# Kernel tuning notes

Measured on AMD Instinct MI355X. Metric: run time of the kernel, lower is better.

## Reference

```python
import math
import jax, jax.numpy as jnp
import numpy as np

STRIDE = 8
IMG = 2048
NA = 9            # num anchors per cell (len(cfg['anchor_size']))
NC = 80           # num classes
TOPK = 1000
CONF = 0.05
NMS_T = 0.6
CTR_CLAMP = 32.0
EXP_CLAMP = math.log(1e8)            # DEFAULT_EXP_CLAMP
SCALE_CLAMP = math.log(1000.0 / 16)  # DEFAULT_SCALE_CLAMP


def setup_inputs() -> dict:
    key = jax.random.key(0)
    k1, k2, k3 = jax.random.split(key, 3)
    H = W = IMG // STRIDE  # 256
    obj_pred = jax.random.normal(k1, (1, NA, H, W), jnp.float32)
    cls_pred = jax.random.normal(k2, (1, NA * NC, H, W), jnp.float32)
    reg_pred = jax.random.normal(k3, (1, NA * 4, H, W), jnp.float32) * 0.5
    # generate_anchors: grid centers (+0.5)*stride, tiled anchor sizes -> [H*W*NA, 4] (cx,cy,w,h)
    ys, xs = jnp.meshgrid(jnp.arange(H), jnp.arange(W), indexing='ij')
    xy = (jnp.stack([xs, ys], -1).reshape(-1, 2).astype(jnp.float32) + 0.5) * STRIDE
    sizes = jnp.array([[32, 32], [64, 64], [128, 128], [32, 64], [64, 128],
                       [128, 256], [64, 32], [128, 64], [256, 128]], jnp.float32)
    anchor_boxes = jnp.concatenate(
        [jnp.repeat(xy[:, None, :], NA, axis=1),
         jnp.broadcast_to(sizes[None], (H * W, NA, 2))], axis=-1).reshape(-1, 4)
    return {"obj_pred": obj_pred, "cls_pred": cls_pred,
            "reg_pred": reg_pred, "anchor_boxes": anchor_boxes}


def _detect(obj_pred, cls_pred, reg_pred, anchor_boxes):
    B, _, H, W = obj_pred.shape
    obj = obj_pred.reshape(B, NA, 1, H, W)
    cls = cls_pred.reshape(B, NA, NC, H, W)
    # normalized_cls_pred = cls + obj - log(1 + exp(clamp(cls)) + exp(clamp(obj)))
    norm = cls + obj - jnp.log(1.0 + jnp.exp(jnp.minimum(cls, EXP_CLAMP))
                               + jnp.exp(jnp.minimum(obj, EXP_CLAMP)))
    norm = norm.transpose(0, 3, 4, 1, 2).reshape(B, -1, NC)[0]          # [M, NC]
    reg = reg_pred.reshape(B, NA, 4, H, W).transpose(0, 3, 4, 1, 2).reshape(B, -1, 4)[0]  # [M, 4]
    prob = jax.nn.sigmoid(norm)
    scores_all = prob.max(axis=-1)
    labels_all = prob.argmax(axis=-1)
    scores, idx = jax.lax.top_k(scores_all, TOPK)                        # descending
    labels = labels_all[idx]
    reg = reg[idx]
    anc = anchor_boxes[idx]
    # decode_boxes
    ctr_off = jnp.clip(reg[..., :2] * anc[..., 2:], -CTR_CLAMP, CTR_CLAMP)
    ctr = anc[..., :2] + ctr_off
    wh = anc[..., 2:] * jnp.exp(jnp.minimum(reg[..., 2:], SCALE_CLAMP))
    boxes = jnp.concatenate([ctr - 0.5 * wh, ctr + 0.5 * wh], axis=-1)
    boxes = jnp.clip(boxes / IMG, 0.0, 1.0)
    return scores, labels, boxes


def _nms_keep(scores, labels, boxes):
    # scores are sorted descending; per-class greedy NMS == class-masked global greedy NMS
    valid = scores >= CONF
    x1, y1, x2, y2 = boxes[:, 0], boxes[:, 1], boxes[:, 2], boxes[:, 3]
    areas = (x2 - x1) * (y2 - y1)
    xx1 = jnp.maximum(x1[:, None], x1[None, :])
    yy1 = jnp.maximum(y1[:, None], y1[None, :])
    xx2 = jnp.minimum(x2[:, None], x2[None, :])
    yy2 = jnp.minimum(y2[:, None], y2[None, :])
    inter = jnp.maximum(1e-28, xx2 - xx1) * jnp.maximum(1e-28, yy2 - yy1)
    iou = inter / (areas[:, None] + areas[None, :] - inter + 1e-14)      # [N, N]
    sup = (iou > NMS_T) & (labels[:, None] == labels[None, :])
    later = jnp.arange(TOPK)[None, :] > jnp.arange(TOPK)[:, None]

    def body(i, keep):
        row = sup[i] & later[i] & keep[i]   # i suppresses only if still kept
        return keep & ~row

    return jax.lax.fori_loop(0, TOPK, body, valid)


def reference(obj_pred, cls_pred, reg_pred, anchor_boxes):
    scores, labels, boxes = _detect(obj_pred, cls_pred, reg_pred, anchor_boxes)
    keep = _nms_keep(scores, labels, boxes)
    # fixed-shape outputs: detections sorted by score with a keep mask
    return scores, labels, boxes, keep
```

## Files before the change

### kernel.cpp

```cpp
#include <hip/hip_runtime.h>
#include <stdint.h>

#define NA 9
#define NC 80
#define NTOT 589824
#define NT4  147456
#define TOPK 1000
#define CONF 0.05f
#define NMS_T 0.6
#define CTR_CLAMP 32.0
#define IMGF 2048.0
#define SCALE_CLAMP 4.135166556742356

#define HIST_OFF   4718592u
#define CNT_OFF    4784128u
#define BARC_OFF   4784384u
#define FLAG_OFF   4792576u
#define INITF_OFF  4800768u
#define CAND_OFF   4802816u
#define BOXES_OFF  4835584u
#define LABS_OFF   4851584u
#define SUPB_OFF   4855584u

#define NBLK 512
#define PER_BLK 288
#define SPIN_CAP 200000
#define INIT_MAGIC 0x9E3779B97F4A7C15ull

__device__ __forceinline__ void stg32(unsigned* p, unsigned v) {
  __hip_atomic_store(p, v, __ATOMIC_RELAXED, __HIP_MEMORY_SCOPE_AGENT);
}
__device__ __forceinline__ unsigned ldg32(const unsigned* p) {
  return __hip_atomic_load((unsigned*)p, __ATOMIC_RELAXED, __HIP_MEMORY_SCOPE_AGENT);
}
__device__ __forceinline__ void stg64(unsigned long long* p, unsigned long long v) {
  __hip_atomic_store(p, v, __ATOMIC_RELAXED, __HIP_MEMORY_SCOPE_AGENT);
}
__device__ __forceinline__ unsigned long long ldg64(const unsigned long long* p) {
  return __hip_atomic_load((unsigned long long*)p, __ATOMIC_RELAXED,
                           __HIP_MEMORY_SCOPE_AGENT);
}

__device__ __forceinline__ unsigned* lslot(unsigned* base, int idx) {
  return (unsigned*)((char*)base + (size_t)idx * 256u);
}

__device__ __forceinline__ void barrier_sync(unsigned* cnts, unsigned* flags,
                                             int b, int bid, unsigned target,
                                             bool i_arrive) {
  __syncthreads();
  if (threadIdx.x == 0) {
    if (i_arrive)
      __hip_atomic_fetch_add(lslot(cnts, b * 8 + (bid & 7)), 1u, __ATOMIC_RELAXED,
                             __HIP_MEMORY_SCOPE_AGENT);
    if (bid == 0) {
      for (int it = 0; it < SPIN_CAP; it++) {
        unsigned s = 0;
#pragma unroll
        for (int i = 0; i < 8; i++)
          s += __hip_atomic_load(lslot(cnts, b * 8 + i), __ATOMIC_RELAXED,
                                 __HIP_MEMORY_SCOPE_AGENT);
        if (s >= target) break;
        __builtin_amdgcn_s_sleep(2);
      }
#pragma unroll
      for (int i = 0; i < 8; i++)
        __hip_atomic_store(lslot(flags, b * 8 + i), 1u, __ATOMIC_RELAXED,
                           __HIP_MEMORY_SCOPE_AGENT);
    } else {
      for (int it = 0; it < SPIN_CAP; it++) {
        if (__hip_atomic_load(lslot(flags, b * 8 + (bid & 7)), __ATOMIC_RELAXED,
                              __HIP_MEMORY_SCOPE_AGENT) != 0u)
          break;
        __builtin_amdgcn_s_sleep(2);
      }
    }
  }
  __syncthreads();
  asm volatile("" ::: "memory");
}

__device__ __forceinline__ float cexpf(float x) {
#pragma clang fp contract(off)
  float m = floorf(__builtin_fmaf(x, 1.44269504088896341f, 0.5f));
  float r = __builtin_fmaf(m, -0.693359375f, x);
  r = __builtin_fmaf(m, 2.12194440e-4f, r);
  float r2 = r * r;
  float y = 1.9875691500E-4f;
  y = __builtin_fmaf(y, r, 1.3981999507E-3f);
  y = __builtin_fmaf(y, r, 8.3334519073E-3f);
  y = __builtin_fmaf(y, r, 4.1665795894E-2f);
  y = __builtin_fmaf(y, r, 1.6666665459E-1f);
  y = __builtin_fmaf(y, r, 5.0000001201E-1f);
  y = __builtin_fmaf(y, r2, r) + 1.0f;
  return ldexpf(y, (int)m);
}

__device__ __forceinline__ float clogf_(float xin) {
#pragma clang fp contract(off)
  unsigned b = __float_as_uint(xin);
  int e = (int)(b >> 23) - 126;
  float m = __uint_as_float((b & 0x007FFFFFu) | 0x3F000000u);
  if (m < 0.707106781186547524f) { e -= 1; m = m + m; }
  float x = m - 1.0f;
  float z = x * x;
  float y = 7.0376836292E-2f;
  y = __builtin_fmaf(y, x, -1.1514610310E-1f);
  y = __builtin_fmaf(y, x, 1.1676998740E-1f);
  y = __builtin_fmaf(y, x, -1.2420140846E-1f);
  y = __builtin_fmaf(y, x, 1.4249322787E-1f);
  y = __builtin_fmaf(y, x, -1.6668057665E-1f);
  y = __builtin_fmaf(y, x, 2.0000714765E-1f);
  y = __builtin_fmaf(y, x, -2.4999993993E-1f);
  y = __builtin_fmaf(y, x, 3.3333331174E-1f);
  y = y * x * z;
  float ef = (float)e;
  y = __builtin_fmaf(ef, -2.12194440e-4f, y);
  y = __builtin_fmaf(-0.5f, z, y);
  float res = x + y;
  res = __builtin_fmaf(ef, 0.693359375f, res);
  return res;
}

__device__ __forceinline__ unsigned long long shflxor64(unsigned long long v, int m) {
  unsigned lo = __shfl_xor((unsigned)v, m, 64);
  unsigned hi = __shfl_xor((unsigned)(v >> 32), m, 64);
  return ((unsigned long long)hi << 32) | lo;
}

__device__ __forceinline__ void score4(const float4* __restrict__ obj4,
                                       const float4* __restrict__ cls4,
                                       unsigned t4, unsigned bv[4], int bc[4],
                                       unsigned* lh) {
#pragma clang fp contract(off)
  int a = (int)(t4 >> 14);
  int rem = (int)(t4 & 16383u);
  float4 ov = obj4[t4];
  float ob[4] = {ov.x, ov.y, ov.z, ov.w};
  float best[4] = {-1e30f, -1e30f, -1e30f, -1e30f};
  bc[0] = bc[1] = bc[2] = bc[3] = 0;
  const float4* cp = cls4 + a * 80 * 16384 + rem;
#pragma unroll 8
  for (int c = 0; c < 80; c++) {
    float4 cv = cp[c * 16384];
    float cl[4] = {cv.x, cv.y, cv.z, cv.w};
#pragma unroll
    for (int k = 0; k < 4; k++) {
      if (cl[k] > best[k]) { best[k] = cl[k]; bc[k] = c; }
    }
  }
#pragma unroll
  for (int k = 0; k < 4; k++) {
    float c = best[k], o = ob[k];
    float ec = cexpf(c);
    float eo = cexpf(o);
    float L = clogf_((1.0f + ec) + eo);
    float nrm = (c + o) - L;
    float p = 1.0f / (1.0f + cexpf(-nrm));
    bv[k] = __float_as_uint(p);
    atomicAdd(&lh[bv[k] >> 16], 1u);
  }
}

__global__ __launch_bounds__(256) void k_fused(
    const float4* __restrict__ obj4, const float4* __restrict__ cls4,
    unsigned* __restrict__ hist, const float* __restrict__ reg_pred,
    const float* __restrict__ anchors, unsigned* __restrict__ cand_cnt,
    unsigned* __restrict__ barc, unsigned* __restrict__ flags,
    unsigned* __restrict__ initf, unsigned long long* __restrict__ cand,
    float* __restrict__ out, float* __restrict__ boxes_s,
    int* __restrict__ labels_s, unsigned long long* __restrict__ supB) {
  int tid = threadIdx.x;
  int bid = blockIdx.x;

  __shared__ __align__(16) unsigned lh[16384];

  for (int i = tid; i < 16384; i += 256) lh[i] = 0u;
  if (bid == 0) {
    for (int i = tid; i < 16384; i += 256) stg32(&hist[i], 0u);
    if (tid == 0) stg32(cand_cnt, 0u);
    if (tid < 32) {
      stg32(lslot(barc, tid), 0u);
      stg32(lslot(flags, tid), 0u);
    }
  }
  __syncthreads();
  if (bid == 0 && tid < 8)
    stg64((unsigned long long*)lslot(initf, tid), INIT_MAGIC);

  int lane = tid & 63, wv = tid >> 6;
  unsigned t4a = (unsigned)bid * PER_BLK + (unsigned)tid;
  unsigned t4b = (unsigned)bid * PER_BLK + 256u + (unsigned)(wv * 8 + lane);
  bool has1 = (lane < 8);
  unsigned bv0[4], bv1[4] = {0, 0, 0, 0};
  int bc0[4], bc1[4] = {0, 0, 0, 0};
  score4(obj4, cls4, t4a, bv0, bc0, lh);
  if (has1) score4(obj4, cls4, t4b, bv1, bc1, lh);

  __syncthreads();
  if (tid == 0) {
    for (int it = 0; it < SPIN_CAP; it++) {
      if (ldg64((unsigned long long*)lslot(initf, bid & 7)) == INIT_MAGIC) break;
      __builtin_amdgcn_s_sleep(2);
    }
  }
  __syncthreads();
  for (int b = tid; b < 16384; b += 256) {
    unsigned v = lh[b];
    if (v) atomicAdd(&hist[b], v);
  }
  barrier_sync(barc, flags, 0, bid, NBLK, true);

  unsigned cB;
  {
    unsigned base = (unsigned)tid * 64u;
    unsigned s = 0;
#pragma unroll 8
    for (int b = 0; b < 64; b++) s += hist[base + b];
    unsigned v = s;
    lh[tid] = v;
    __syncthreads();
    for (int off = 1; off < 256; off <<= 1) {
      unsigned add = (tid + off < 256) ? lh[tid + off] : 0u;
      __syncthreads();
      v += add;
      lh[tid] = v;
      __syncthreads();
    }
    unsigned nxt = (tid < 255) ? lh[tid + 1] : 0u;
    if (v >= TOPK && nxt < TOPK) { lh[260] = (unsigned)tid; lh[261] = nxt; }
    __syncthreads();
    unsigned C = lh[260];
    unsigned above = lh[261];
    if (tid < 64) {
      unsigned h = hist[C * 64u + (unsigned)tid];
      unsigned acc = h;
      for (int off = 1; off < 64; off <<= 1) {
        unsigned o = __shfl_down(acc, off, 64);
        if (tid + off < 64) acc += o;
      }
      acc += above;
      if (acc >= TOPK && (tid == 63 || (acc - h) < TOPK))
        lh[262] = C * 64u + (unsigned)tid;
    }
    __syncthreads();
    cB = lh[262];
  }

  {
#pragma unroll
    for (int k = 0; k < 4; k++) {
      bool win = (bv0[k] >> 16) >= cB;
      unsigned long long m = __ballot(win);
      if (m != 0ull) {
        int leader = __ffsll((long long)m) - 1;
        unsigned base2 = 0;
        if (lane == leader) base2 = atomicAdd(cand_cnt, (unsigned)__popcll(m));
        base2 = __shfl(base2, leader, 64);
        if (win) {
          unsigned w = 4u * t4a + (unsigned)k;
          unsigned a = w >> 16, hw = w & 65535u;
          unsigned j = hw * 9u + a;
          unsigned pos = base2 + (unsigned)__popcll(m & ((1ull << lane) - 1ull));
          if (pos < 4096u)
            stg64(&cand[pos], ((unsigned long long)bv0[k] << 27) |
                                  ((unsigned long long)(0xFFFFFu - j) << 7) |
                                  (unsigned long long)(unsigned)bc0[k]);
        }
      }
    }
#pragma unroll
    for (int k = 0; k < 4; k++) {
      bool win = has1 && ((bv1[k] >> 16) >= cB);
      unsigned long long m = __ballot(win);
      if (m != 0ull) {
        int leader = __ffsll((long long)m) - 1;
        unsigned base2 = 0;
        if (lane == leader) base2 = atomicAdd(cand_cnt, (unsigned)__popcll(m));
        base2 = __shfl(base2, leader, 64);
        if (win) {
          unsigned w = 4u * t4b + (unsigned)k;
          unsigned a = w >> 16, hw = w & 65535u;
          unsigned j = hw * 9u + a;
          unsigned pos = base2 + (unsigned)__popcll(m & ((1ull << lane) - 1ull));
          if (pos < 4096u)
            stg64(&cand[pos], ((unsigned long long)bv1[k] << 27) |
                                  ((unsigned long long)(0xFFFFFu - j) << 7) |
                                  (unsigned long long)(unsigned)bc1[k]);
        }
      }
    }
  }
  barrier_sync(barc, flags, 1, bid, NBLK, true);

  if (bid < 16) {
    unsigned long long* s_key = (unsigned long long*)lh;
    int c = bid * 256 + tid;
    unsigned M = ldg32(cand_cnt);
    if (M > 4096u) M = 4096u;
    unsigned long long mykey = (c < (int)M) ? ldg64(&cand[c]) : 0ull;
    unsigned rank = 0;
    int ntile = (int)((M + 255u) >> 8);
    for (int tile = 0; tile < ntile; tile++) {
      __syncthreads();
      int src = tile * 256 + tid;
      s_key[tid] = (src < (int)M) ? ldg64(&cand[src]) : 0ull;
      __syncthreads();
#pragma unroll 8
      for (int q = 0; q < 256; q++) rank += (s_key[q] > mykey) ? 1u : 0u;
    }
    if (c < (int)M && rank < TOPK) {
      int r = (int)rank;
      int lab = (int)(mykey & 0x7Full);
      unsigned j = 0xFFFFFu - (unsigned)((mykey >> 7) & 0xFFFFFull);
      unsigned hw = j / 9u;
      unsigned a = j - hw * 9u;
      unsigned base = a * 4u * 65536u + hw;
      double r0 = (double)reg_pred[base];
      double r1 = (double)reg_pred[base + 65536u];
      double r2 = (double)reg_pred[base + 131072u];
      double r3 = (double)reg_pred[base + 196608u];
      double ax = (double)anchors[j * 4u + 0], ay = (double)anchors[j * 4u + 1];
      double aw = (double)anchors[j * 4u + 2], ah = (double)anchors[j * 4u + 3];
      double ox = fmin(fmax(r0 * aw, -CTR_CLAMP), CTR_CLAMP);
      double oy = fmin(fmax(r1 * ah, -CTR_CLAMP), CTR_CLAMP);
      double cx = ax + ox, cy = ay + oy;
      double ww = aw * exp(fmin(r2, SCALE_CLAMP));
      double hh = ah * exp(fmin(r3, SCALE_CLAMP));
      float x1 = (float)fmin(fmax((cx - 0.5 * ww) * (1.0 / IMGF), 0.0), 1.0);
      float y1 = (float)fmin(fmax((cy - 0.5 * hh) * (1.0 / IMGF), 0.0), 1.0);
      float x2 = (float)fmin(fmax((cx + 0.5 * ww) * (1.0 / IMGF), 0.0), 1.0);
      float y2 = (float)fmin(fmax((cy + 0.5 * hh) * (1.0 / IMGF), 0.0), 1.0);
      out[1000 + r] = (float)lab;
      out[2000 + 4 * r + 0] = x1;
      out[2000 + 4 * r + 1] = y1;
      out[2000 + 4 * r + 2] = x2;
      out[2000 + 4 * r + 3] = y2;
      stg32((unsigned*)&out[r], (unsigned)(mykey >> 27));
      stg32((unsigned*)&boxes_s[4 * r + 0], __float_as_uint(x1));
      stg32((unsigned*)&boxes_s[4 * r + 1], __float_as_uint(y1));
      stg32((unsigned*)&boxes_s[4 * r + 2], __float_as_uint(x2));
      stg32((unsigned*)&boxes_s[4 * r + 3], __float_as_uint(y2));
      stg32((unsigned*)&labels_s[r], (unsigned)lab);
    }
  }
  barrier_sync(barc, flags, 2, bid, 16, bid < 16);

  {
    float* s_bx = (float*)lh;
    int* s_lb = (int*)((char*)lh + 16000);
    for (int t = tid; t < 4000; t += 256)
      s_bx[t] = __uint_as_float(ldg32((const unsigned*)&boxes_s[t]));
    for (int t = tid; t < 1000; t += 256)
      s_lb[t] = (int)ldg32((const unsigned*)&labels_s[t]);
    __syncthreads();
    for (int half = 0; half < 2; half++) {
      int i = bid + half * NBLK;
      if (i < TOPK) {
        double ix1 = (double)s_bx[4 * i], iy1 = (double)s_bx[4 * i + 1];
        double ix2 = (double)s_bx[4 * i + 2], iy2 = (double)s_bx[4 * i + 3];
        double ia = (ix2 - ix1) * (iy2 - iy1);
        int il = s_lb[i];
        for (int rep = 0; rep < 4; rep++) {
          int j = rep * 256 + tid;
          bool s = false;
          if (j < TOPK && j > i && s_lb[j] == il) {
            double jx1 = (double)s_bx[4 * j], jy1 = (double)s_bx[4 * j + 1];
            double jx2 = (double)s_bx[4 * j + 2], jy2 = (double)s_bx[4 * j + 3];
            double xx1 = fmax(ix1, jx1), yy1 = fmax(iy1, jy1);
            double xx2 = fmin(ix2, jx2), yy2 = fmin(iy2, jy2);
            double inter = fmax(1e-28, xx2 - xx1) * fmax(1e-28, yy2 - yy1);
            double ja = (jx2 - jx1) * (jy2 - jy1);
            double iou = inter / (ia + ja - inter + 1e-14);
            s = iou > NMS_T;
          }
          unsigned long long w = __ballot(s);
          if ((tid & 63) == 0)
            stg64(&supB[(rep * 4 + (tid >> 6)) * 1024 + i], w);
        }
      }
    }
  }
  __syncthreads();
  if (tid == 0)
    __hip_atomic_fetch_add(lslot(barc, 3 * 8 + (bid & 7)), 1u, __ATOMIC_RELAXED,
                           __HIP_MEMORY_SCOPE_AGENT);
  if (bid != 0) return;
  if (tid == 0) {
    for (int it = 0; it < SPIN_CAP; it++) {
      unsigned s = 0;
#pragma unroll
      for (int i = 0; i < 8; i++)
        s += __hip_atomic_load(lslot(barc, 3 * 8 + i), __ATOMIC_RELAXED,
                               __HIP_MEMORY_SCOPE_AGENT);
      if (s >= NBLK) break;
      __builtin_amdgcn_s_sleep(2);
    }
  }
  __syncthreads();
  asm volatile("" ::: "memory");

  if (tid < 64) {
    float* keep_out = out + 6000;
    unsigned long long inval[16];
#pragma unroll
    for (int m = 0; m < 16; m++) {
      int j = m * 64 + lane;
      bool bad = (j >= TOPK) ||
                 (__uint_as_float(ldg32((const unsigned*)&out[j])) < CONF);
      inval[m] = __ballot(bad);
    }
    unsigned long long kept[16];
#pragma unroll
    for (int b = 0; b < 16; b++) {
      unsigned long long acc = 0ull;
#pragma unroll
      for (int m = 0; m < b; m++) {
        unsigned long long r = ldg64(&supB[b * 1024 + m * 64 + lane]);
        if ((kept[m] >> lane) & 1ull) acc |= r;
      }
      if (b > 0) {
#pragma unroll
        for (int s = 1; s < 64; s <<= 1) acc |= shflxor64(acc, s);
      }
      unsigned alo = __builtin_amdgcn_readfirstlane((unsigned)acc);
      unsigned ahi = __builtin_amdgcn_readfirstlane((unsigned)(acc >> 32));
      unsigned long long cur = inval[b] | (((unsigned long long)ahi << 32) | alo);
      unsigned long long diag = ldg64(&supB[b * 1024 + b * 64 + lane]);
      unsigned dlo = (unsigned)diag, dhi = (unsigned)(diag >> 32);
#pragma unroll 8
      for (int k = 0; k < 64; k++) {
        unsigned rlo = __builtin_amdgcn_readlane(dlo, k);
        unsigned rhi = __builtin_amdgcn_readlane(dhi, k);
        unsigned long long rk = ((unsigned long long)rhi << 32) | rlo;
        unsigned long long take = ((cur >> k) & 1ull) ? 0ull : rk;
        cur |= take;
      }
      kept[b] = ~cur;
    }
#pragma unroll
    for (int m = 0; m < 16; m++) {
      int j = m * 64 + lane;
      if (j < TOPK) keep_out[j] = ((kept[m] >> lane) & 1ull) ? 1.0f : 0.0f;
    }
  }
}

extern "C" void kernel_launch(void* const* d_in, const int* in_sizes, int n_in,
                              void* d_out, int out_size, void* d_ws, size_t ws_size,
                              hipStream_t stream) {
  const float* obj = (const float*)d_in[0];
  const float* cls = (const float*)d_in[1];
  const float* reg = (const float*)d_in[2];
  const float* anc = (const float*)d_in[3];
  float* out = (float*)d_out;
  char* ws = (char*)d_ws;

  const float4* obj4 = (const float4*)obj;
  const float4* cls4 = (const float4*)cls;
  unsigned* hist = (unsigned*)(ws + HIST_OFF);
  unsigned* cand_cnt = (unsigned*)(ws + CNT_OFF);
  unsigned* barc = (unsigned*)(ws + BARC_OFF);
  unsigned* flags = (unsigned*)(ws + FLAG_OFF);
  unsigned* initf = (unsigned*)(ws + INITF_OFF);
  unsigned long long* cand = (unsigned long long*)(ws + CAND_OFF);
  float* boxes_s = (float*)(ws + BOXES_OFF);
  int* labels_s = (int*)(ws + LABS_OFF);
  unsigned long long* supB = (unsigned long long*)(ws + SUPB_OFF);

  void* kargs[] = {(void*)&obj4,  (void*)&cls4,     (void*)&hist,
                   (void*)&reg,   (void*)&anc,      (void*)&cand_cnt,
                   (void*)&barc,  (void*)&flags,    (void*)&initf,
                   (void*)&cand,  (void*)&out,      (void*)&boxes_s,
                   (void*)&labels_s, (void*)&supB};
  hipLaunchCooperativeKernel((const void*)k_fused, dim3(NBLK), dim3(256), kargs, 0,
                             stream);
}
```

Measured before the change: 400.3 us.

## Pack LDS histogram into 16-bit pairs, raise occupancy, and prefetch class loads

Halves the per-block LDS histogram by packing two 16-bit bin counts per word, so more blocks fit per CU. The grid size is now chosen at runtime from the occupancy query, and work is distributed with a strided multi-item loop. The 80-class argmax loop is software-pipelined with double-buffered float4 loads to hide memory latency. The extra prefetch registers may limit occupancy, and 16-bit counters could overflow if a block ever puts 65536 items in one bin.

```diff
diff --git a/kernel.cpp b/kernel.cpp
--- a/kernel.cpp
+++ b/kernel.cpp
@@ -22,8 +22,6 @@
 #define LABS_OFF   4851584u
 #define SUPB_OFF   4855584u
 
-#define NBLK 512
-#define PER_BLK 288
 #define SPIN_CAP 200000
 #define INIT_MAGIC 0x9E3779B97F4A7C15ull
 
@@ -140,13 +138,25 @@
   float best[4] = {-1e30f, -1e30f, -1e30f, -1e30f};
   bc[0] = bc[1] = bc[2] = bc[3] = 0;
   const float4* cp = cls4 + a * 80 * 16384 + rem;
-#pragma unroll 8
-  for (int c = 0; c < 80; c++) {
-    float4 cv = cp[c * 16384];
-    float cl[4] = {cv.x, cv.y, cv.z, cv.w};
-#pragma unroll
-    for (int k = 0; k < 4; k++) {
-      if (cl[k] > best[k]) { best[k] = cl[k]; bc[k] = c; }
+  float4 va[8], vb[8];
+#pragma unroll
+  for (int u = 0; u < 8; u++) va[u] = cp[u * 16384];
+#pragma unroll
+  for (int s = 0; s < 10; s++) {
+    const float4* src = (s & 1) ? vb : va;
+    float4* dst = (s & 1) ? va : vb;
+    if (s < 9) {
+#pragma unroll
+      for (int u = 0; u < 8; u++) dst[u] = cp[((s + 1) * 8 + u) * 16384];
+    }
+#pragma unroll
+    for (int u = 0; u < 8; u++) {
+      int c = s * 8 + u;
+      float cl[4] = {src[u].x, src[u].y, src[u].z, src[u].w};
+#pragma unroll
+      for (int k = 0; k < 4; k++) {
+        if (cl[k] > best[k]) { best[k] = cl[k]; bc[k] = c; }
+      }
     }
   }
 #pragma unroll
@@ -158,11 +168,11 @@
     float nrm = (c + o) - L;
     float p = 1.0f / (1.0f + cexpf(-nrm));
     bv[k] = __float_as_uint(p);
-    atomicAdd(&lh[bv[k] >> 16], 1u);
-  }
-}
-
-__global__ __launch_bounds__(256) void k_fused(
+    atomicAdd(&lh[bv[k] >> 17], 1u << (((bv[k] >> 16) & 1u) * 16u));
+  }
+}
+
+__global__ __launch_bounds__(256, 3) void k_fused(
     const float4* __restrict__ obj4, const float4* __restrict__ cls4,
     unsigned* __restrict__ hist, const float* __restrict__ reg_pred,
     const float* __restrict__ anchors, unsigned* __restrict__ cand_cnt,
@@ -172,10 +182,12 @@
     int* __restrict__ labels_s, unsigned long long* __restrict__ supB) {
   int tid = threadIdx.x;
   int bid = blockIdx.x;
-
-  __shared__ __align__(16) unsigned lh[16384];
-
-  for (int i = tid; i < 16384; i += 256) lh[i] = 0u;
+  int lane = tid & 63;
+  unsigned nblk = gridDim.x;
+
+  __shared__ __align__(16) unsigned lh[8192];
+
+  for (int i = tid; i < 8192; i += 256) lh[i] = 0u;
   if (bid == 0) {
     for (int i = tid; i < 16384; i += 256) stg32(&hist[i], 0u);
     if (tid == 0) stg32(cand_cnt, 0u);
@@ -188,14 +200,17 @@
   if (bid == 0 && tid < 8)
     stg64((unsigned long long*)lslot(initf, tid), INIT_MAGIC);
 
-  int lane = tid & 63, wv = tid >> 6;
-  unsigned t4a = (unsigned)bid * PER_BLK + (unsigned)tid;
-  unsigned t4b = (unsigned)bid * PER_BLK + 256u + (unsigned)(wv * 8 + lane);
-  bool has1 = (lane < 8);
-  unsigned bv0[4], bv1[4] = {0, 0, 0, 0};
-  int bc0[4], bc1[4] = {0, 0, 0, 0};
-  score4(obj4, cls4, t4a, bv0, bc0, lh);
-  if (has1) score4(obj4, cls4, t4b, bv1, bc1, lh);
+  unsigned bvA[3][4];
+  int bcA[3][4];
+  unsigned tA[3];
+  bool vld[3];
+#pragma unroll
+  for (int it = 0; it < 3; it++) {
+    unsigned t4 = (unsigned)bid * 256u + (unsigned)tid + (unsigned)it * nblk * 256u;
+    tA[it] = t4;
+    vld[it] = (t4 < (unsigned)NT4);
+    if (vld[it]) score4(obj4, cls4, t4, bvA[it], bcA[it], lh);
+  }
 
   __syncthreads();
   if (tid == 0) {
@@ -205,11 +220,12 @@
     }
   }
   __syncthreads();
-  for (int b = tid; b < 16384; b += 256) {
-    unsigned v = lh[b];
-    if (v) atomicAdd(&hist[b], v);
-  }
-  barrier_sync(barc, flags, 0, bid, NBLK, true);
+  for (int b = tid; b < 8192; b += 256) {
+    unsigned w = lh[b];
+    if (w & 0xFFFFu) atomicAdd(&hist[2 * b], w & 0xFFFFu);
+    if (w >> 16) atomicAdd(&hist[2 * b + 1], w >> 16);
+  }
+  barrier_sync(barc, flags, 0, bid, nblk, true);
 
   unsigned cB;
   {
@@ -249,49 +265,31 @@
 
   {
 #pragma unroll
-    for (int k = 0; k < 4; k++) {
-      bool win = (bv0[k] >> 16) >= cB;
-      unsigned long long m = __ballot(win);
-      if (m != 0ull) {
-        int leader = __ffsll((long long)m) - 1;
-        unsigned base2 = 0;
-        if (lane == leader) base2 = atomicAdd(cand_cnt, (unsigned)__popcll(m));
-        base2 = __shfl(base2, leader, 64);
-        if (win) {
-          unsigned w = 4u * t4a + (unsigned)k;
-          unsigned a = w >> 16, hw = w & 65535u;
-          unsigned j = hw * 9u + a;
-          unsigned pos = base2 + (unsigned)__popcll(m & ((1ull << lane) - 1ull));
-          if (pos < 4096u)
-            stg64(&cand[pos], ((unsigned long long)bv0[k] << 27) |
-                                  ((unsigned long long)(0xFFFFFu - j) << 7) |
-                                  (unsigned long long)(unsigned)bc0[k]);
+    for (int it = 0; it < 3; it++) {
+#pragma unroll
+      for (int k = 0; k < 4; k++) {
+        bool win = vld[it] && ((bvA[it][k] >> 16) >= cB);
+        unsigned long long m = __ballot(win);
+        if (m != 0ull) {
+          int leader = __ffsll((long long)m) - 1;
+          unsigned base2 = 0;
+          if (lane == leader) base2 = atomicAdd(cand_cnt, (unsigned)__popcll(m));
+          base2 = __shfl(base2, leader, 64);
+          if (win) {
+            unsigned w = 4u * tA[it] + (unsigned)k;
+            unsigned a = w >> 16, hw = w & 65535u;
+            unsigned j = hw * 9u + a;
+            unsigned pos = base2 + (unsigned)__popcll(m & ((1ull << lane) - 1ull));
+            if (pos < 4096u)
+              stg64(&cand[pos], ((unsigned long long)bvA[it][k] << 27) |
+                                    ((unsigned long long)(0xFFFFFu - j) << 7) |
+                                    (unsigned long long)(unsigned)bcA[it][k]);
+          }
         }
       }
     }
-#pragma unroll
-    for (int k = 0; k < 4; k++) {
-      bool win = has1 && ((bv1[k] >> 16) >= cB);
-      unsigned long long m = __ballot(win);
-      if (m != 0ull) {
-        int leader = __ffsll((long long)m) - 1;
-        unsigned base2 = 0;
-        if (lane == leader) base2 = atomicAdd(cand_cnt, (unsigned)__popcll(m));
-        base2 = __shfl(base2, leader, 64);
-        if (win) {
-          unsigned w = 4u * t4b + (unsigned)k;
-          unsigned a = w >> 16, hw = w & 65535u;
-          unsigned j = hw * 9u + a;
-          unsigned pos = base2 + (unsigned)__popcll(m & ((1ull << lane) - 1ull));
-          if (pos < 4096u)
-            stg64(&cand[pos], ((unsigned long long)bv1[k] << 27) |
-                                  ((unsigned long long)(0xFFFFFu - j) << 7) |
-                                  (unsigned long long)(unsigned)bc1[k]);
-        }
-      }
-    }
-  }
-  barrier_sync(barc, flags, 1, bid, NBLK, true);
+  }
+  barrier_sync(barc, flags, 1, bid, nblk, true);
 
   if (bid < 16) {
     unsigned long long* s_key = (unsigned long long*)lh;
@@ -354,30 +352,27 @@
     for (int t = tid; t < 1000; t += 256)
       s_lb[t] = (int)ldg32((const unsigned*)&labels_s[t]);
     __syncthreads();
-    for (int half = 0; half < 2; half++) {
-      int i = bid + half * NBLK;
-      if (i < TOPK) {
-        double ix1 = (double)s_bx[4 * i], iy1 = (double)s_bx[4 * i + 1];
-        double ix2 = (double)s_bx[4 * i + 2], iy2 = (double)s_bx[4 * i + 3];
-        double ia = (ix2 - ix1) * (iy2 - iy1);
-        int il = s_lb[i];
-        for (int rep = 0; rep < 4; rep++) {
-          int j = rep * 256 + tid;
-          bool s = false;
-          if (j < TOPK && j > i && s_lb[j] == il) {
-            double jx1 = (double)s_bx[4 * j], jy1 = (double)s_bx[4 * j + 1];
-            double jx2 = (double)s_bx[4 * j + 2], jy2 = (double)s_bx[4 * j + 3];
-            double xx1 = fmax(ix1, jx1), yy1 = fmax(iy1, jy1);
-            double xx2 = fmin(ix2, jx2), yy2 = fmin(iy2, jy2);
-            double inter = fmax(1e-28, xx2 - xx1) * fmax(1e-28, yy2 - yy1);
-            double ja = (jx2 - jx1) * (jy2 - jy1);
-            double iou = inter / (ia + ja - inter + 1e-14);
-            s = iou > NMS_T;
-          }
-          unsigned long long w = __ballot(s);
-          if ((tid & 63) == 0)
-            stg64(&supB[(rep * 4 + (tid >> 6)) * 1024 + i], w);
+    for (int i = bid; i < TOPK; i += (int)nblk) {
+      double ix1 = (double)s_bx[4 * i], iy1 = (double)s_bx[4 * i + 1];
+      double ix2 = (double)s_bx[4 * i + 2], iy2 = (double)s_bx[4 * i + 3];
+      double ia = (ix2 - ix1) * (iy2 - iy1);
+      int il = s_lb[i];
+      for (int rep = 0; rep < 4; rep++) {
+        int j = rep * 256 + tid;
+        bool s = false;
+        if (j < TOPK && j > i && s_lb[j] == il) {
+          double jx1 = (double)s_bx[4 * j], jy1 = (double)s_bx[4 * j + 1];
+          double jx2 = (double)s_bx[4 * j + 2], jy2 = (double)s_bx[4 * j + 3];
+          double xx1 = fmax(ix1, jx1), yy1 = fmax(iy1, jy1);
+          double xx2 = fmin(ix2, jx2), yy2 = fmin(iy2, jy2);
+          double inter = fmax(1e-28, xx2 - xx1) * fmax(1e-28, yy2 - yy1);
+          double ja = (jx2 - jx1) * (jy2 - jy1);
+          double iou = inter / (ia + ja - inter + 1e-14);
+          s = iou > NMS_T;
         }
+        unsigned long long w = __ballot(s);
+        if ((tid & 63) == 0)
+          stg64(&supB[(rep * 4 + (tid >> 6)) * 1024 + i], w);
       }
     }
   }
@@ -393,7 +388,7 @@
       for (int i = 0; i < 8; i++)
         s += __hip_atomic_load(lslot(barc, 3 * 8 + i), __ATOMIC_RELAXED,
                                __HIP_MEMORY_SCOPE_AGENT);
-      if (s >= NBLK) break;
+      if (s >= nblk) break;
       __builtin_amdgcn_s_sleep(2);
     }
   }
@@ -468,11 +463,18 @@
   int* labels_s = (int*)(ws + LABS_OFF);
   unsigned long long* supB = (unsigned long long*)(ws + SUPB_OFF);
 
+  int maxb = 0;
+  if (hipOccupancyMaxActiveBlocksPerMultiprocessor(&maxb, k_fused, 256, 0) !=
+          hipSuccess ||
+      maxb <= 0)
+    maxb = 2;
+  int nblk = (maxb >= 3) ? 576 : ((maxb >= 2) ? 512 : 256);
+
   void* kargs[] = {(void*)&obj4,  (void*)&cls4,     (void*)&hist,
                    (void*)&reg,   (void*)&anc,      (void*)&cand_cnt,
                    (void*)&barc,  (void*)&flags,    (void*)&initf,
                    (void*)&cand,  (void*)&out,      (void*)&boxes_s,
                    (void*)&labels_s, (void*)&supB};
-  hipLaunchCooperativeKernel((const void*)k_fused, dim3(NBLK), dim3(256), kargs, 0,
+  hipLaunchCooperativeKernel((const void*)k_fused, dim3(nblk), dim3(256), kargs, 0,
                              stream);
 }
```

Measured after the change: 395.5 us. About the same (-1.2%).
